# Optimization experiments

Hardware: AMD Instinct MI355X
Metric: run time of the kernel (lower is better)

The kernel has to match this reference:

```python
import jax, jax.numpy as jnp
import numpy as np

NEG_SLOPE = 0.2


def gat_conv(x, src, dst, W, a_src, a_dst, b, concat):
    # x: [N, Fin]; W: [H*C, Fin]; a_src/a_dst: [H, C]; b: [H*C] or [C]
    N = x.shape[0]
    H, C = a_src.shape
    h = (x @ W.T).reshape(N, H, C)                      # per-head transform
    s_n = jnp.sum(h * a_src, axis=-1)                   # [N, H]
    d_n = jnp.sum(h * a_dst, axis=-1)                   # [N, H]
    e = jax.nn.leaky_relu(s_n[src] + d_n[dst], NEG_SLOPE)  # [E, H]
    # segment softmax over incoming edges of each destination node
    m = jax.ops.segment_max(e, dst, num_segments=N)
    m = jnp.where(jnp.isfinite(m), m, 0.0)
    ex = jnp.exp(e - m[dst])
    denom = jax.ops.segment_sum(ex, dst, num_segments=N)
    alpha = ex / (denom[dst] + 1e-16)                    # [E, H]
    msg = h[src] * alpha[:, :, None]                     # [E, H, C]
    out = jax.ops.segment_sum(msg, dst, num_segments=N)  # [N, H, C]
    out = out.reshape(N, H * C) if concat else out.mean(axis=1)
    return out + b


def setup_inputs() -> dict:
    key = jax.random.key(0)
    ks = jax.random.split(key, 16)
    N, E, F, C, H = 50000, 800000, 256, 128, 4
    sc = lambda fan_in: 1.0 / np.sqrt(fan_in)
    inp = {
        "x": jax.random.normal(ks[0], (N, F), dtype=jnp.float32),
        "edge_index": jax.random.randint(ks[1], (2, E), 0, N, dtype=jnp.int64),
        # layer 1: F -> H*C (concat)
        "W1": jax.random.normal(ks[2], (H * C, F), jnp.float32) * sc(F),
        "a_src1": jax.random.normal(ks[3], (H, C), jnp.float32) * sc(C),
        "a_dst1": jax.random.normal(ks[4], (H, C), jnp.float32) * sc(C),
        "b1": jnp.zeros((H * C,), jnp.float32),
        # layer 2: H*C -> H*C (concat)
        "W2": jax.random.normal(ks[5], (H * C, H * C), jnp.float32) * sc(H * C),
        "a_src2": jax.random.normal(ks[6], (H, C), jnp.float32) * sc(C),
        "a_dst2": jax.random.normal(ks[7], (H, C), jnp.float32) * sc(C),
        "b2": jnp.zeros((H * C,), jnp.float32),
        # layer 3: H*C -> C (heads=1, concat=False)
        "W3": jax.random.normal(ks[8], (C, H * C), jnp.float32) * sc(H * C),
        "a_src3": jax.random.normal(ks[9], (1, C), jnp.float32) * sc(C),
        "a_dst3": jax.random.normal(ks[10], (1, C), jnp.float32) * sc(C),
        "b3": jnp.zeros((C,), jnp.float32),
        # allocation head: C -> C//2 -> 1
        "Wh1": jax.random.normal(ks[11], (C // 2, C), jnp.float32) * sc(C),
        "bh1": jnp.zeros((C // 2,), jnp.float32),
        "Wh2": jax.random.normal(ks[12], (1, C // 2), jnp.float32) * sc(C // 2),
        "bh2": jnp.zeros((1,), jnp.float32),
    }
    return inp


def reference(x, edge_index, W1, a_src1, a_dst1, b1, W2, a_src2, a_dst2, b2,
              W3, a_src3, a_dst3, b3, Wh1, bh1, Wh2, bh2):
    N = x.shape[0]
    loops = jnp.arange(N, dtype=edge_index.dtype)
    src = jnp.concatenate([edge_index[0], loops])  # self-loops (PyG default)
    dst = jnp.concatenate([edge_index[1], loops])

    h = gat_conv(x, src, dst, W1, a_src1, a_dst1, b1, concat=True)
    h = jax.nn.elu(h)  # dropout is identity at inference
    h = gat_conv(h, src, dst, W2, a_src2, a_dst2, b2, concat=True)
    h = jax.nn.elu(h)
    embeddings = gat_conv(h, src, dst, W3, a_src3, a_dst3, b3, concat=False)

    z = jax.nn.relu(embeddings @ Wh1.T + bh1)
    allocation_scores = jax.nn.sigmoid(z @ Wh2.T + bh2)
    return embeddings, allocation_scores
```

## Files before the change

kernel.cpp:

```cpp
#include <hip/hip_runtime.h>
#include <math.h>

typedef _Float16 f16;
typedef f16 f16x2 __attribute__((ext_vector_type(2)));
typedef f16 f16x8 __attribute__((ext_vector_type(8)));
typedef float f32x4 __attribute__((ext_vector_type(4)));

template <int V> struct VecT;
template <> struct VecT<2> { using T = f16 __attribute__((ext_vector_type(2))); };
template <> struct VecT<8> { using T = f16 __attribute__((ext_vector_type(8))); };

__device__ __forceinline__ unsigned ordf(float f) {
  unsigned u = __float_as_uint(f);
  return (u >> 31) ? ~u : (u | 0x80000000u);
}
__device__ __forceinline__ float unordf(unsigned u) {
  return (u >> 31) ? __uint_as_float(u & 0x7fffffffu) : __uint_as_float(~u);
}


__global__ void k_count(const int* __restrict__ dstArr, int* __restrict__ cnt,
                        int E, int Et) {
  int i = blockIdx.x * blockDim.x + threadIdx.x;
  if (i >= Et) return;
  int d = (i < E) ? dstArr[i] : (i - E);
  atomicAdd(&cnt[d], 1);
}

__global__ __launch_bounds__(256) void k_scanA(const int* __restrict__ cnt,
                                               int* __restrict__ row_ptr,
                                               int* __restrict__ bsum, int n) {
  __shared__ int part[256];
  int t = threadIdx.x;
  int base = blockIdx.x * 1024 + t * 4;
  int4 v = make_int4(0, 0, 0, 0);
  if (base + 3 < n) v = *(const int4*)&cnt[base];
  else {
    if (base + 0 < n) v.x = cnt[base + 0];
    if (base + 1 < n) v.y = cnt[base + 1];
    if (base + 2 < n) v.z = cnt[base + 2];
    if (base + 3 < n) v.w = cnt[base + 3];
  }
  int s = v.x + v.y + v.z + v.w;
  part[t] = s;
  __syncthreads();
  for (int off = 1; off < 256; off <<= 1) {
    int x = (t >= off) ? part[t - off] : 0;
    __syncthreads();
    part[t] += x;
    __syncthreads();
  }
  int p0 = (t == 0) ? 0 : part[t - 1];
  int p1 = p0 + v.x, p2 = p1 + v.y, p3 = p2 + v.z;
  if (base + 0 < n) row_ptr[base + 0] = p0;
  if (base + 1 < n) row_ptr[base + 1] = p1;
  if (base + 2 < n) row_ptr[base + 2] = p2;
  if (base + 3 < n) row_ptr[base + 3] = p3;
  if (t == 255) bsum[blockIdx.x] = part[255];
}

__global__ __launch_bounds__(1024) void k_scanB(int* __restrict__ bsum, int nb) {
  __shared__ int part[1024];
  int t = threadIdx.x;
  int v = (t < nb) ? bsum[t] : 0;
  part[t] = v;
  __syncthreads();
  for (int off = 1; off < 1024; off <<= 1) {
    int x = (t >= off) ? part[t - off] : 0;
    __syncthreads();
    part[t] += x;
    __syncthreads();
  }
  if (t < nb) bsum[t] = (t == 0) ? 0 : part[t - 1];
  if (t == 1023) bsum[nb] = part[1023];
}

__global__ void k_scanC(int* __restrict__ row_ptr, int* __restrict__ cursor,
                        const int* __restrict__ bsum, int n, int nb) {
  int i = blockIdx.x * blockDim.x + threadIdx.x;
  if (i < n) {
    int v = row_ptr[i] + bsum[i >> 10];
    row_ptr[i] = v;
    cursor[i] = v;
  }
  if (i == n) row_ptr[n] = bsum[nb];
}

__global__ void k_fill(const int* __restrict__ dstArr, int* __restrict__ cursor,
                       int* __restrict__ perm, int E, int Et) {
  int i = blockIdx.x * blockDim.x + threadIdx.x;
  if (i >= Et) return;
  int d = (i < E) ? dstArr[i] : (i - E);
  int pos = atomicAdd(&cursor[d], 1);
  perm[pos] = i;
}

__global__ void k_f2h4(const float* s0, f16* d0, int n0,
                       const float* s1, f16* d1, int n1,
                       const float* s2, f16* d2, int n2,
                       const float* s3, f16* d3, int n3) {
  int i = blockIdx.x * blockDim.x + threadIdx.x;
  const float* s; f16* d;
  if (i < n0) { s = s0; d = d0; }
  else if ((i -= n0) < n1) { s = s1; d = d1; }
  else if ((i -= n1) < n2) { s = s2; d = d2; }
  else if ((i -= n2) < n3) { s = s3; d = d3; }
  else return;
  float4 v = ((const float4*)s)[i];
  union { f16 h[4]; double dd; } u;
  u.h[0] = (f16)v.x; u.h[1] = (f16)v.y; u.h[2] = (f16)v.z; u.h[3] = (f16)v.w;
  ((double*)d)[i] = u.dd;
}

__global__ __launch_bounds__(256) void k_hgemm_nt(
    const f16* __restrict__ A, const f16* __restrict__ B,
    f16* __restrict__ C, int M, int Nn, int K,
    const float* __restrict__ a_src, const float* __restrict__ a_dst,
    float* __restrict__ sArr, float* __restrict__ dArr,
    unsigned* __restrict__ gmaxU, int H) {
  __shared__ f16 As[128 * 32];
  __shared__ f16 Bs[128 * 32];
  int tid = threadIdx.x;
  int wave = tid >> 6, lane = tid & 63;
  int quad = lane >> 4, l16 = lane & 15;
  int m0 = blockIdx.y * 128, n0 = blockIdx.x * 128;
  int wm = (wave & 1) * 64, wn = (wave >> 1) * 64;

  int lr = lane >> 2;
  int lc = lane & 3;
  int chunk = lc ^ ((lr >> 1) & 3);
  int rb0 = wave * 16;
  int rb1 = 64 + wave * 16;
  int ga0 = m0 + rb0 + lr; if (ga0 >= M) ga0 = M - 1;
  int ga1 = m0 + rb1 + lr; if (ga1 >= M) ga1 = M - 1;
  const f16* gA0 = A + (size_t)ga0 * K + chunk * 8;
  const f16* gA1 = A + (size_t)ga1 * K + chunk * 8;
  const f16* gB0 = B + (size_t)(n0 + rb0 + lr) * K + chunk * 8;
  const f16* gB1 = B + (size_t)(n0 + rb1 + lr) * K + chunk * 8;
  f16* lA0 = &As[rb0 * 32];
  f16* lA1 = &As[rb1 * 32];
  f16* lB0 = &Bs[rb0 * 32];
  f16* lB1 = &Bs[rb1 * 32];

  int rsw = (quad ^ ((l16 >> 1) & 3)) * 8;
  const f16* Ard[4];
  const f16* Brd[4];
#pragma unroll
  for (int i = 0; i < 4; ++i) {
    Ard[i] = &As[(wm + i * 16 + l16) * 32 + rsw];
    Brd[i] = &Bs[(wn + i * 16 + l16) * 32 + rsw];
  }

  f32x4 acc[4][4];
#pragma unroll
  for (int i = 0; i < 4; ++i)
#pragma unroll
    for (int j = 0; j < 4; ++j) acc[i][j] = (f32x4)(0.f);

  for (int k0 = 0; k0 < K; k0 += 32) {
    __syncthreads();
    __builtin_amdgcn_global_load_lds(
        (const __attribute__((address_space(1))) void*)(gA0 + k0),
        (__attribute__((address_space(3))) void*)lA0, 16, 0, 0);
    __builtin_amdgcn_global_load_lds(
        (const __attribute__((address_space(1))) void*)(gA1 + k0),
        (__attribute__((address_space(3))) void*)lA1, 16, 0, 0);
    __builtin_amdgcn_global_load_lds(
        (const __attribute__((address_space(1))) void*)(gB0 + k0),
        (__attribute__((address_space(3))) void*)lB0, 16, 0, 0);
    __builtin_amdgcn_global_load_lds(
        (const __attribute__((address_space(1))) void*)(gB1 + k0),
        (__attribute__((address_space(3))) void*)lB1, 16, 0, 0);
    __syncthreads();
    f16x8 af[4], bf[4];
#pragma unroll
    for (int i = 0; i < 4; ++i) af[i] = *(const f16x8*)Ard[i];
#pragma unroll
    for (int j = 0; j < 4; ++j) bf[j] = *(const f16x8*)Brd[j];
#pragma unroll
    for (int i = 0; i < 4; ++i)
#pragma unroll
      for (int j = 0; j < 4; ++j)
        acc[i][j] = __builtin_amdgcn_mfma_f32_16x16x32_f16(af[i], bf[j], acc[i][j], 0, 0, 0);
  }

#pragma unroll
  for (int i = 0; i < 4; ++i) {
#pragma unroll
    for (int r = 0; r < 4; ++r) {
      int m = m0 + wm + i * 16 + quad * 4 + r;
      if (m < M) {
        f16* Cp = C + (size_t)m * Nn + n0 + wn + l16;
#pragma unroll
        for (int j = 0; j < 4; ++j) Cp[j * 16] = (f16)acc[i][j][r];
      }
    }
  }

  float av[4], ad[4];
#pragma unroll
  for (int j = 0; j < 4; ++j) {
    int col = n0 + wn + l16 + j * 16;
    av[j] = a_src[col];
    ad[j] = a_dst[col];
  }
  float sp[16], dp[16];
#pragma unroll
  for (int i = 0; i < 4; ++i)
#pragma unroll
    for (int r = 0; r < 4; ++r) {
      float ss = 0.f, dd = 0.f;
#pragma unroll
      for (int j = 0; j < 4; ++j) {
        ss += acc[i][j][r] * av[j];
        dd += acc[i][j][r] * ad[j];
      }
#pragma unroll
      for (int msk = 1; msk < 16; msk <<= 1) {
        ss += __shfl_xor(ss, msk);
        dd += __shfl_xor(dd, msk);
      }
      sp[i * 4 + r] = ss;
      dp[i * 4 + r] = dd;
    }

  __syncthreads();
  float* fb = (float*)As;
  int wv = wn >> 6;
  if (l16 == 0) {
#pragma unroll
    for (int i = 0; i < 4; ++i)
#pragma unroll
      for (int r = 0; r < 4; ++r) {
        int row = wm + i * 16 + quad * 4 + r;
        fb[wv * 128 + row] = sp[i * 4 + r];
        fb[256 + wv * 128 + row] = dp[i * 4 + r];
      }
  }
  __syncthreads();
  if (tid < 128) {
    int m = m0 + tid;
    if (m < M) {
      float s = fb[tid] + fb[128 + tid];
      float d = fb[256 + tid] + fb[384 + tid];
      int head = n0 >> 7;
      sArr[(size_t)m * H + head] = s;
      dArr[(size_t)m * H + head] = d;
      atomicMax(&gmaxU[head], ordf(s));
    }
  }
}

template <int HH, int CT, bool DOELU, typename OutT>
__global__ __launch_bounds__(256) void k_aggregate(
    const f16* __restrict__ hin, const float* __restrict__ sArr,
    const float* __restrict__ dArr, const int* __restrict__ row_ptr,
    const int* __restrict__ perm, const int* __restrict__ srcArr,
    const unsigned* __restrict__ gmaxU, const float* __restrict__ bias,
    OutT* __restrict__ outp, int N, int E) {
  constexpr int VEC = CT / 64;
  constexpr int CPER = CT / HH;
  using gvec = typename VecT<VEC>::T;

  int n = blockIdx.x * 4 + (threadIdx.x >> 6);
  int lane = threadIdx.x & 63;
  if (n >= N) return;
  int e0 = row_ptr[n];
  int deg = row_ptr[n + 1] - e0;

  float dloc[HH], mn[HH];
#pragma unroll
  for (int h = 0; h < HH; ++h) {
    dloc[h] = dArr[n * HH + h];
    float m = unordf(gmaxU[h]) + dloc[h];
    mn[h] = (m > 0.f) ? m : 0.2f * m;
  }

  const int lanehead = (HH == 1) ? 0 : (lane * VEC) / CPER;
  float acc[VEC];
#pragma unroll
  for (int k = 0; k < VEC; ++k) acc[k] = 0.f;
  float denom[HH];
#pragma unroll
  for (int h = 0; h < HH; ++h) denom[h] = 0.f;

  for (int base = 0; base < deg; base += 64) {
    int cn = min(64, deg - base);
    int s_l = n;
    float w_l[HH];
#pragma unroll
    for (int h = 0; h < HH; ++h) w_l[h] = 0.f;
    if (lane < cn) {
      int eid = perm[e0 + base + lane];
      s_l = (eid < E) ? srcArr[eid] : (eid - E);
      if (HH == 4) {
        float4 sv = ((const float4*)sArr)[s_l];
        float svv[4] = {sv.x, sv.y, sv.z, sv.w};
#pragma unroll
        for (int h = 0; h < 4; ++h) {
          float e = svv[h] + dloc[h];
          e = (e > 0.f) ? e : 0.2f * e;
          w_l[h] = __expf(e - mn[h]);
        }
      } else {
        float e = sArr[s_l] + dloc[0];
        e = (e > 0.f) ? e : 0.2f * e;
        w_l[0] = __expf(e - mn[0]);
      }
    }
    for (int i = 0; i < cn; ++i) {
      int s = __shfl(s_l, i);
      float wh[HH];
#pragma unroll
      for (int h = 0; h < HH; ++h) {
        wh[h] = __shfl(w_l[h], i);
        denom[h] += wh[h];
      }
      float w = wh[lanehead];
      gvec v = *(const gvec*)(hin + (size_t)s * CT + lane * VEC);
#pragma unroll
      for (int k = 0; k < VEC; ++k) acc[k] += w * (float)v[k];
    }
  }

  float dn = denom[lanehead] + 1e-16f;
  struct alignas(sizeof(OutT) * VEC) OutV { OutT v[VEC]; } ov;
#pragma unroll
  for (int k = 0; k < VEC; ++k) {
    float v = acc[k] / dn + bias[lane * VEC + k];
    if (DOELU) v = (v > 0.f) ? v : expm1f(v);
    ov.v[k] = (OutT)v;
  }
  *(OutV*)(outp + (size_t)n * CT + lane * VEC) = ov;
}

__global__ __launch_bounds__(256) void k_head(
    const float* __restrict__ emb, const float* __restrict__ Wh1,
    const float* __restrict__ bh1, const float* __restrict__ Wh2,
    const float* __restrict__ bh2, float* __restrict__ scores, int N) {
  __shared__ float w1s[64 * 132];
  __shared__ float w2s[64];
  __shared__ float b1s[64];
  int t = threadIdx.x;
  for (int i = t; i < 64 * 32; i += 256) {
    int r = i >> 5, c4 = i & 31;
    float4 v = ((const float4*)Wh1)[i];
    *(float4*)&w1s[r * 132 + c4 * 4] = v;
  }
  if (t < 64) { w2s[t] = Wh2[t]; b1s[t] = bh1[t]; }
  __syncthreads();
  float b2v = bh2[0];
  int wave = t >> 6, lane = t & 63;
  int gw = blockIdx.x * 4 + wave;
  int nw = gridDim.x * 4;
  for (int n = gw; n < N; n += nw) {
    float2 xv = ((const float2*)(emb + (size_t)n * 128))[lane];
    float z = b1s[lane];
#pragma unroll
    for (int j = 0; j < 32; ++j) {
      float4 w = *(const float4*)&w1s[lane * 132 + 4 * j];
      float a0 = __shfl(xv.x, 2 * j);
      float a1 = __shfl(xv.y, 2 * j);
      float a2 = __shfl(xv.x, 2 * j + 1);
      float a3 = __shfl(xv.y, 2 * j + 1);
      z += w.x * a0 + w.y * a1 + w.z * a2 + w.w * a3;
    }
    z = fmaxf(z, 0.f);
    float v = z * w2s[lane];
#pragma unroll
    for (int off = 32; off; off >>= 1) v += __shfl_down(v, off);
    if (lane == 0) scores[n] = 1.f / (1.f + __expf(-(v + b2v)));
  }
}


extern "C" void kernel_launch(void* const* d_in, const int* in_sizes, int n_in,
                              void* d_out, int out_size, void* d_ws, size_t ws_size,
                              hipStream_t stream) {
  const float* x   = (const float*)d_in[0];
  const int*   ei  = (const int*)d_in[1];
  const float* W1  = (const float*)d_in[2];
  const float* as1 = (const float*)d_in[3];
  const float* ad1 = (const float*)d_in[4];
  const float* b1  = (const float*)d_in[5];
  const float* W2  = (const float*)d_in[6];
  const float* as2 = (const float*)d_in[7];
  const float* ad2 = (const float*)d_in[8];
  const float* b2  = (const float*)d_in[9];
  const float* W3  = (const float*)d_in[10];
  const float* as3 = (const float*)d_in[11];
  const float* ad3 = (const float*)d_in[12];
  const float* b3  = (const float*)d_in[13];
  const float* Wh1 = (const float*)d_in[14];
  const float* bh1 = (const float*)d_in[15];
  const float* Wh2 = (const float*)d_in[16];
  const float* bh2 = (const float*)d_in[17];
  float* out = (float*)d_out;

  const int F = 256, HC = 512, H = 4, C = 128;
  const int N = in_sizes[0] / F;
  const int E = in_sizes[1] / 2;
  const int Et = E + N;
  const int* srcArr = ei;
  const int* dstArr = ei + E;

  char* ws = (char*)d_ws;
  size_t off = 0;
  auto alloc = [&](size_t bytes) -> void* {
    void* p = ws + off;
    off += (bytes + 255) & ~(size_t)255;
    return p;
  };
  f16*   h16    = (f16*)alloc((size_t)N * HC * 2);
  f16*   hAgg   = (f16*)alloc((size_t)N * HC * 2);
  f16*   xh     = (f16*)alloc((size_t)N * F * 2);
  f16*   W1h    = (f16*)alloc((size_t)HC * F * 2);
  f16*   W2h    = (f16*)alloc((size_t)HC * HC * 2);
  f16*   W3h    = (f16*)alloc((size_t)C * HC * 2);
  int* row_ptr  = (int*)alloc((size_t)(N + 1) * 4);
  char* zr      = (char*)alloc((size_t)N * 4 + 64);
  int* cnt      = (int*)zr;
  unsigned* gm1 = (unsigned*)(zr + (size_t)N * 4);
  unsigned* gm2 = gm1 + 4;
  unsigned* gm3 = gm1 + 8;
  int* cursor   = (int*)alloc((size_t)N * 4);
  int* perm     = (int*)alloc((size_t)Et * 4);
  float* sArr   = (float*)alloc((size_t)N * H * 4);
  float* dArr   = (float*)alloc((size_t)N * H * 4);
  int* bsum     = (int*)alloc((size_t)1028 * 4);
  (void)ws_size; (void)n_in; (void)out_size;

  hipMemsetAsync(zr, 0, (size_t)N * 4 + 64, stream);
  int eb = (Et + 255) / 256;
  int nb = (N + 1023) / 1024;
  k_count<<<eb, 256, 0, stream>>>(dstArr, cnt, E, Et);
  k_scanA<<<nb, 256, 0, stream>>>(cnt, row_ptr, bsum, N);
  k_scanB<<<1, 1024, 0, stream>>>(bsum, nb);
  k_scanC<<<(N + 256) / 256, 256, 0, stream>>>(row_ptr, cursor, bsum, N, nb);
  k_fill<<<eb, 256, 0, stream>>>(dstArr, cursor, perm, E, Et);

  int c0 = N * F / 4, c1 = HC * F / 4, c2 = HC * HC / 4, c3 = C * HC / 4;
  int ctot = c0 + c1 + c2 + c3;
  k_f2h4<<<(ctot + 255) / 256, 256, 0, stream>>>(x, xh, c0, W1, W1h, c1,
                                                 W2, W2h, c2, W3, W3h, c3);

  int aggGrid = (N + 3) / 4;
  dim3 g1(HC / 128, (N + 127) / 128);
  dim3 g3(C / 128, (N + 127) / 128);

  k_hgemm_nt<<<g1, 256, 0, stream>>>(xh, W1h, h16, N, HC, F,
                                     as1, ad1, sArr, dArr, gm1, H);
  k_aggregate<4, 512, true, f16><<<aggGrid, 256, 0, stream>>>(
      h16, sArr, dArr, row_ptr, perm, srcArr, gm1, b1, hAgg, N, E);

  k_hgemm_nt<<<g1, 256, 0, stream>>>(hAgg, W2h, h16, N, HC, HC,
                                     as2, ad2, sArr, dArr, gm2, H);
  k_aggregate<4, 512, true, f16><<<aggGrid, 256, 0, stream>>>(
      h16, sArr, dArr, row_ptr, perm, srcArr, gm2, b2, hAgg, N, E);

  k_hgemm_nt<<<g3, 256, 0, stream>>>(hAgg, W3h, h16, N, C, HC,
                                     as3, ad3, sArr, dArr, gm3, 1);
  k_aggregate<1, 128, false, float><<<aggGrid, 256, 0, stream>>>(
      h16, sArr, dArr, row_ptr, perm, srcArr, gm3, b3, out, N, E);

  k_head<<<512, 256, 0, stream>>>(out, Wh1, bh1, Wh2, bh2, out + (size_t)N * C, N);
}
```

Baseline: 841.7 us.

## Fuse CSR build into one persistent kernel and convert x inside GEMM

The five CSR-construction kernels (count, three-stage scan, fill) become one 256-block persistent kernel that separates phases with a software grid barrier built on atomics and sleeps. The x-to-fp16 conversion pass is dropped: the first GEMM reads fp32 x directly, converts in registers and writes to LDS instead of using direct global-to-LDS loads. This removes several launches and a full read/write pass over x. In exchange the grid barrier assumes all 256 blocks are co-resident, the scan phases are limited to one block of 256 chunks, and the layer-1 A-tile path doubles global read bytes and drops the async LDS load.

```diff
diff --git a/kernel.cpp b/kernel.cpp
--- a/kernel.cpp
+++ b/kernel.cpp
@@ -18,93 +18,103 @@
   return (u >> 31) ? __uint_as_float(u & 0x7fffffffu) : __uint_as_float(~u);
 }
 
-
-__global__ void k_count(const int* __restrict__ dstArr, int* __restrict__ cnt,
-                        int E, int Et) {
-  int i = blockIdx.x * blockDim.x + threadIdx.x;
-  if (i >= Et) return;
-  int d = (i < E) ? dstArr[i] : (i - E);
-  atomicAdd(&cnt[d], 1);
-}
-
-__global__ __launch_bounds__(256) void k_scanA(const int* __restrict__ cnt,
-                                               int* __restrict__ row_ptr,
-                                               int* __restrict__ bsum, int n) {
+__device__ __forceinline__ f16x8 cvt8(float4 a, float4 b) {
+  f16x8 r;
+  r[0] = (f16)a.x; r[1] = (f16)a.y; r[2] = (f16)a.z; r[3] = (f16)a.w;
+  r[4] = (f16)b.x; r[5] = (f16)b.y; r[6] = (f16)b.z; r[7] = (f16)b.w;
+  return r;
+}
+
+__device__ __forceinline__ void gridbar(int* arrive, int ph) {
+  __syncthreads();
+  if (threadIdx.x == 0) {
+    __threadfence();
+    atomicAdd(arrive, 1);
+    int target = ph * (int)gridDim.x;
+    while (atomicAdd(arrive, 0) < target) __builtin_amdgcn_s_sleep(2);
+    __threadfence();
+  }
+  __syncthreads();
+}
+
+__global__ __launch_bounds__(256) void k_csr(
+    const int* __restrict__ dstArr, int* cnt, int* row_ptr, int* cursor,
+    int* __restrict__ perm, int* bsum, int* arrive,
+    int n, int E, int Et, int nch) {
   __shared__ int part[256];
   int t = threadIdx.x;
-  int base = blockIdx.x * 1024 + t * 4;
-  int4 v = make_int4(0, 0, 0, 0);
-  if (base + 3 < n) v = *(const int4*)&cnt[base];
-  else {
-    if (base + 0 < n) v.x = cnt[base + 0];
-    if (base + 1 < n) v.y = cnt[base + 1];
-    if (base + 2 < n) v.z = cnt[base + 2];
-    if (base + 3 < n) v.w = cnt[base + 3];
-  }
-  int s = v.x + v.y + v.z + v.w;
-  part[t] = s;
-  __syncthreads();
-  for (int off = 1; off < 256; off <<= 1) {
-    int x = (t >= off) ? part[t - off] : 0;
+  int b = blockIdx.x;
+  int gid = b * 256 + t;
+  int gsz = gridDim.x * 256;
+
+  for (int i = gid; i < Et; i += gsz) {
+    int d = (i < E) ? dstArr[i] : (i - E);
+    atomicAdd(&cnt[d], 1);
+  }
+  gridbar(arrive, 1);
+
+  if (b < nch) {
+    int base = b * 1024 + t * 4;
+    int v0 = 0, v1 = 0, v2 = 0, v3 = 0;
+    if (base + 0 < n) v0 = atomicAdd(&cnt[base + 0], 0);
+    if (base + 1 < n) v1 = atomicAdd(&cnt[base + 1], 0);
+    if (base + 2 < n) v2 = atomicAdd(&cnt[base + 2], 0);
+    if (base + 3 < n) v3 = atomicAdd(&cnt[base + 3], 0);
+    part[t] = v0 + v1 + v2 + v3;
     __syncthreads();
-    part[t] += x;
+    for (int off = 1; off < 256; off <<= 1) {
+      int x = (t >= off) ? part[t - off] : 0;
+      __syncthreads();
+      part[t] += x;
+      __syncthreads();
+    }
+    int p0 = (t == 0) ? 0 : part[t - 1];
+    if (base + 0 < n) atomicExch(&row_ptr[base + 0], p0);
+    if (base + 1 < n) atomicExch(&row_ptr[base + 1], p0 + v0);
+    if (base + 2 < n) atomicExch(&row_ptr[base + 2], p0 + v0 + v1);
+    if (base + 3 < n) atomicExch(&row_ptr[base + 3], p0 + v0 + v1 + v2);
+    if (t == 255) atomicExch(&bsum[b], part[255]);
+  }
+  gridbar(arrive, 2);
+
+  if (b == 0) {
+    int v = (t < nch) ? atomicAdd(&bsum[t], 0) : 0;
+    part[t] = v;
     __syncthreads();
-  }
-  int p0 = (t == 0) ? 0 : part[t - 1];
-  int p1 = p0 + v.x, p2 = p1 + v.y, p3 = p2 + v.z;
-  if (base + 0 < n) row_ptr[base + 0] = p0;
-  if (base + 1 < n) row_ptr[base + 1] = p1;
-  if (base + 2 < n) row_ptr[base + 2] = p2;
-  if (base + 3 < n) row_ptr[base + 3] = p3;
-  if (t == 255) bsum[blockIdx.x] = part[255];
-}
-
-__global__ __launch_bounds__(1024) void k_scanB(int* __restrict__ bsum, int nb) {
-  __shared__ int part[1024];
-  int t = threadIdx.x;
-  int v = (t < nb) ? bsum[t] : 0;
-  part[t] = v;
-  __syncthreads();
-  for (int off = 1; off < 1024; off <<= 1) {
-    int x = (t >= off) ? part[t - off] : 0;
-    __syncthreads();
-    part[t] += x;
-    __syncthreads();
-  }
-  if (t < nb) bsum[t] = (t == 0) ? 0 : part[t - 1];
-  if (t == 1023) bsum[nb] = part[1023];
-}
-
-__global__ void k_scanC(int* __restrict__ row_ptr, int* __restrict__ cursor,
-                        const int* __restrict__ bsum, int n, int nb) {
-  int i = blockIdx.x * blockDim.x + threadIdx.x;
-  if (i < n) {
-    int v = row_ptr[i] + bsum[i >> 10];
-    row_ptr[i] = v;
-    cursor[i] = v;
-  }
-  if (i == n) row_ptr[n] = bsum[nb];
-}
-
-__global__ void k_fill(const int* __restrict__ dstArr, int* __restrict__ cursor,
-                       int* __restrict__ perm, int E, int Et) {
-  int i = blockIdx.x * blockDim.x + threadIdx.x;
-  if (i >= Et) return;
-  int d = (i < E) ? dstArr[i] : (i - E);
-  int pos = atomicAdd(&cursor[d], 1);
-  perm[pos] = i;
-}
-
-__global__ void k_f2h4(const float* s0, f16* d0, int n0,
+    for (int off = 1; off < 256; off <<= 1) {
+      int x = (t >= off) ? part[t - off] : 0;
+      __syncthreads();
+      part[t] += x;
+      __syncthreads();
+    }
+    if (t < nch) atomicExch(&bsum[t], (t == 0) ? 0 : part[t - 1]);
+    if (t == 255) atomicExch(&bsum[nch], part[255]);
+  }
+  gridbar(arrive, 3);
+
+  for (int i = gid; i < n; i += gsz) {
+    int bs = atomicAdd(&bsum[i >> 10], 0);
+    int old = atomicAdd(&row_ptr[i], bs);
+    atomicExch(&cursor[i], old + bs);
+  }
+  if (gid == 0) atomicExch(&row_ptr[n], atomicAdd(&bsum[nch], 0));
+  gridbar(arrive, 4);
+
+  for (int i = gid; i < Et; i += gsz) {
+    int d = (i < E) ? dstArr[i] : (i - E);
+    int pos = atomicAdd(&cursor[d], 1);
+    perm[pos] = i;
+  }
+}
+
+__global__ void k_f2h3(const float* s0, f16* d0, int n0,
                        const float* s1, f16* d1, int n1,
-                       const float* s2, f16* d2, int n2,
-                       const float* s3, f16* d3, int n3) {
+                       const float* s2, f16* d2, int n2) {
   int i = blockIdx.x * blockDim.x + threadIdx.x;
   const float* s; f16* d;
   if (i < n0) { s = s0; d = d0; }
   else if ((i -= n0) < n1) { s = s1; d = d1; }
   else if ((i -= n1) < n2) { s = s2; d = d2; }
-  else if ((i -= n2) < n3) { s = s3; d = d3; }
   else return;
   float4 v = ((const float4*)s)[i];
   union { f16 h[4]; double dd; } u;
@@ -112,8 +122,9 @@
   ((double*)d)[i] = u.dd;
 }
 
+template <bool AF32>
 __global__ __launch_bounds__(256) void k_hgemm_nt(
-    const f16* __restrict__ A, const f16* __restrict__ B,
+    const void* __restrict__ Ain, const f16* __restrict__ B,
     f16* __restrict__ C, int M, int Nn, int K,
     const float* __restrict__ a_src, const float* __restrict__ a_dst,
     float* __restrict__ sArr, float* __restrict__ dArr,
@@ -133,14 +144,26 @@
   int rb1 = 64 + wave * 16;
   int ga0 = m0 + rb0 + lr; if (ga0 >= M) ga0 = M - 1;
   int ga1 = m0 + rb1 + lr; if (ga1 >= M) ga1 = M - 1;
-  const f16* gA0 = A + (size_t)ga0 * K + chunk * 8;
-  const f16* gA1 = A + (size_t)ga1 * K + chunk * 8;
+
+  const f16* gA0 = nullptr; const f16* gA1 = nullptr;
+  const float* gA0f = nullptr; const float* gA1f = nullptr;
+  if constexpr (AF32) {
+    const float* Af = (const float*)Ain;
+    gA0f = Af + (size_t)ga0 * K + chunk * 8;
+    gA1f = Af + (size_t)ga1 * K + chunk * 8;
+  } else {
+    const f16* Ah = (const f16*)Ain;
+    gA0 = Ah + (size_t)ga0 * K + chunk * 8;
+    gA1 = Ah + (size_t)ga1 * K + chunk * 8;
+  }
   const f16* gB0 = B + (size_t)(n0 + rb0 + lr) * K + chunk * 8;
   const f16* gB1 = B + (size_t)(n0 + rb1 + lr) * K + chunk * 8;
   f16* lA0 = &As[rb0 * 32];
   f16* lA1 = &As[rb1 * 32];
   f16* lB0 = &Bs[rb0 * 32];
   f16* lB1 = &Bs[rb1 * 32];
+  f16* lwA0 = &As[(rb0 + lr) * 32 + lc * 8];
+  f16* lwA1 = &As[(rb1 + lr) * 32 + lc * 8];
 
   int rsw = (quad ^ ((l16 >> 1) & 3)) * 8;
   const f16* Ard[4];
@@ -158,13 +181,27 @@
     for (int j = 0; j < 4; ++j) acc[i][j] = (f32x4)(0.f);
 
   for (int k0 = 0; k0 < K; k0 += 32) {
+    f16x8 wa0, wa1;
+    if constexpr (AF32) {
+      float4 u00 = *(const float4*)(gA0f + k0);
+      float4 u01 = *(const float4*)(gA0f + k0 + 4);
+      float4 u10 = *(const float4*)(gA1f + k0);
+      float4 u11 = *(const float4*)(gA1f + k0 + 4);
+      wa0 = cvt8(u00, u01);
+      wa1 = cvt8(u10, u11);
+    }
     __syncthreads();
-    __builtin_amdgcn_global_load_lds(
-        (const __attribute__((address_space(1))) void*)(gA0 + k0),
-        (__attribute__((address_space(3))) void*)lA0, 16, 0, 0);
-    __builtin_amdgcn_global_load_lds(
-        (const __attribute__((address_space(1))) void*)(gA1 + k0),
-        (__attribute__((address_space(3))) void*)lA1, 16, 0, 0);
+    if constexpr (AF32) {
+      *(f16x8*)lwA0 = wa0;
+      *(f16x8*)lwA1 = wa1;
+    } else {
+      __builtin_amdgcn_global_load_lds(
+          (const __attribute__((address_space(1))) void*)(gA0 + k0),
+          (__attribute__((address_space(3))) void*)lA0, 16, 0, 0);
+      __builtin_amdgcn_global_load_lds(
+          (const __attribute__((address_space(1))) void*)(gA1 + k0),
+          (__attribute__((address_space(3))) void*)lA1, 16, 0, 0);
+    }
     __builtin_amdgcn_global_load_lds(
         (const __attribute__((address_space(1))) void*)(gB0 + k0),
         (__attribute__((address_space(3))) void*)lB0, 16, 0, 0);
@@ -413,7 +450,6 @@
   };
   f16*   h16    = (f16*)alloc((size_t)N * HC * 2);
   f16*   hAgg   = (f16*)alloc((size_t)N * HC * 2);
-  f16*   xh     = (f16*)alloc((size_t)N * F * 2);
   f16*   W1h    = (f16*)alloc((size_t)HC * F * 2);
   f16*   W2h    = (f16*)alloc((size_t)HC * HC * 2);
   f16*   W3h    = (f16*)alloc((size_t)C * HC * 2);
@@ -423,43 +459,40 @@
   unsigned* gm1 = (unsigned*)(zr + (size_t)N * 4);
   unsigned* gm2 = gm1 + 4;
   unsigned* gm3 = gm1 + 8;
+  int* arrive   = (int*)(gm1 + 12);
   int* cursor   = (int*)alloc((size_t)N * 4);
   int* perm     = (int*)alloc((size_t)Et * 4);
   float* sArr   = (float*)alloc((size_t)N * H * 4);
   float* dArr   = (float*)alloc((size_t)N * H * 4);
-  int* bsum     = (int*)alloc((size_t)1028 * 4);
+  int* bsum     = (int*)alloc((size_t)260 * 4);
   (void)ws_size; (void)n_in; (void)out_size;
 
   hipMemsetAsync(zr, 0, (size_t)N * 4 + 64, stream);
-  int eb = (Et + 255) / 256;
-  int nb = (N + 1023) / 1024;
-  k_count<<<eb, 256, 0, stream>>>(dstArr, cnt, E, Et);
-  k_scanA<<<nb, 256, 0, stream>>>(cnt, row_ptr, bsum, N);
-  k_scanB<<<1, 1024, 0, stream>>>(bsum, nb);
-  k_scanC<<<(N + 256) / 256, 256, 0, stream>>>(row_ptr, cursor, bsum, N, nb);
-  k_fill<<<eb, 256, 0, stream>>>(dstArr, cursor, perm, E, Et);
-
-  int c0 = N * F / 4, c1 = HC * F / 4, c2 = HC * HC / 4, c3 = C * HC / 4;
-  int ctot = c0 + c1 + c2 + c3;
-  k_f2h4<<<(ctot + 255) / 256, 256, 0, stream>>>(x, xh, c0, W1, W1h, c1,
-                                                 W2, W2h, c2, W3, W3h, c3);
+  int nch = (N + 1023) / 1024;
+  k_csr<<<256, 256, 0, stream>>>(dstArr, cnt, row_ptr, cursor, perm, bsum,
+                                 arrive, N, E, Et, nch);
+
+  int c1 = HC * F / 4, c2 = HC * HC / 4, c3 = C * HC / 4;
+  int ctot = c1 + c2 + c3;
+  k_f2h3<<<(ctot + 255) / 256, 256, 0, stream>>>(W1, W1h, c1, W2, W2h, c2,
+                                                 W3, W3h, c3);
 
   int aggGrid = (N + 3) / 4;
   dim3 g1(HC / 128, (N + 127) / 128);
   dim3 g3(C / 128, (N + 127) / 128);
 
-  k_hgemm_nt<<<g1, 256, 0, stream>>>(xh, W1h, h16, N, HC, F,
-                                     as1, ad1, sArr, dArr, gm1, H);
+  k_hgemm_nt<true><<<g1, 256, 0, stream>>>(x, W1h, h16, N, HC, F,
+                                           as1, ad1, sArr, dArr, gm1, H);
   k_aggregate<4, 512, true, f16><<<aggGrid, 256, 0, stream>>>(
       h16, sArr, dArr, row_ptr, perm, srcArr, gm1, b1, hAgg, N, E);
 
-  k_hgemm_nt<<<g1, 256, 0, stream>>>(hAgg, W2h, h16, N, HC, HC,
-                                     as2, ad2, sArr, dArr, gm2, H);
+  k_hgemm_nt<false><<<g1, 256, 0, stream>>>(hAgg, W2h, h16, N, HC, HC,
+                                            as2, ad2, sArr, dArr, gm2, H);
   k_aggregate<4, 512, true, f16><<<aggGrid, 256, 0, stream>>>(
       h16, sArr, dArr, row_ptr, perm, srcArr, gm2, b2, hAgg, N, E);
 
-  k_hgemm_nt<<<g3, 256, 0, stream>>>(hAgg, W3h, h16, N, C, HC,
-                                     as3, ad3, sArr, dArr, gm3, 1);
+  k_hgemm_nt<false><<<g3, 256, 0, stream>>>(hAgg, W3h, h16, N, C, HC,
+                                            as3, ad3, sArr, dArr, gm3, 1);
   k_aggregate<1, 128, false, float><<<aggGrid, 256, 0, stream>>>(
       h16, sArr, dArr, row_ptr, perm, srcArr, gm3, b3, out, N, E);
 
```

Result: slower. 921.4 us (+9.5%).
